# Kernel tuning notes

Measured on AMD Instinct MI355X. Metric: run time of the kernel, lower is better.

The kernel has to match this reference:

```python
import jax, jax.numpy as jnp
import numpy as np

NEG = -1e30  # safe log-zero for fp32/bf16


def _ctc_neg_log_likelihood(labels, log_probs, label_length, data_length, blank):
    """Standard CTC alpha (forward) DP in log space.
    labels: [B, L] int, log_probs: [T, B, C], lengths: [B] int.
    Returns per-example negative log likelihood [B]."""
    T, B, C = log_probs.shape
    L = labels.shape[1]
    S = 2 * L + 1  # extended label: blank, l1, blank, l2, ..., blank
    ext = jnp.full((B, S), blank, dtype=labels.dtype).at[:, 1::2].set(labels)
    prev2 = jnp.concatenate([jnp.full((B, 2), -1, labels.dtype), ext[:, :-2]], axis=1)
    allow_skip = (ext != blank) & (ext != prev2)  # [B, S] skip-transition legality

    def emit(lp_t):  # [B, C] -> [B, S]
        return jnp.take_along_axis(lp_t, ext, axis=1)

    # t = 0: paths can only be at s=0 (blank) or s=1 (first label)
    alpha0 = jnp.where(jnp.arange(S)[None, :] < 2, emit(log_probs[0]), NEG)

    def step(alpha, xs):
        lp_t, t = xs
        a1 = jnp.concatenate([jnp.full((B, 1), NEG, alpha.dtype), alpha[:, :-1]], axis=1)
        a2 = jnp.concatenate([jnp.full((B, 2), NEG, alpha.dtype), alpha[:, :-2]], axis=1)
        a2 = jnp.where(allow_skip, a2, NEG)
        new = jax.nn.logsumexp(jnp.stack([alpha, a1, a2]), axis=0) + emit(lp_t)
        # freeze alpha once past this example's sequence length
        return jnp.where((t < data_length)[:, None], new, alpha), None

    alpha, _ = jax.lax.scan(step, alpha0, (log_probs[1:], jnp.arange(1, T)))

    # likelihood = alpha[2*len] (final blank) + alpha[2*len - 1] (final label)
    a_blank = jnp.take_along_axis(alpha, (2 * label_length)[:, None], axis=1)[:, 0]
    a_label = jnp.take_along_axis(alpha, (2 * label_length - 1)[:, None], axis=1)[:, 0]
    return -jnp.logaddexp(a_blank, a_label)


def setup_inputs() -> dict:
    key = jax.random.key(0)
    k1, k2, k3, k4 = jax.random.split(key, 4)
    T, B, C, L = 1024, 32, 1024, 128
    data = jax.random.normal(k1, (T, B, C), dtype=jnp.float32)
    labels = jax.random.randint(k2, (B, L), 1, C, dtype=jnp.int32)  # avoid blank=0
    label_length = jax.random.randint(k3, (B,), 64, L + 1, dtype=jnp.int32)
    data_length = jax.random.randint(k4, (B,), 512, T + 1, dtype=jnp.int32)
    return {"labels": labels, "data": data, "label_length": label_length,
            "data_length": data_length}


def reference(labels, data, label_length, data_length):
    # from_logits=True -> ctc_loss_v2: log_softmax then CTC; blank_index=0
    log_probs = jax.nn.log_softmax(data, axis=-1)
    loss = _ctc_neg_log_likelihood(labels, log_probs, label_length, data_length, 0)
    return jnp.mean(loss).reshape([1])
```

## Files before the change

kernel.cpp:

```cpp
#include <hip/hip_runtime.h>
#include <hip/hip_bf16.h>

#define T_DIM 1024
#define B_DIM 32
#define C_DIM 1024
#define L_DIM 128
#define S_DIM 257
#define CH    32

#define WS_EPAIR   0
#define WS_LNB     (32u * 1024u * 64u * 8u)
#define WS_ALPHA   (WS_LNB + 32u * 1024u * 4u)
#define WS_BETA    (WS_ALPHA + 32u * 264u * 8u)
#define WS_KACC    (WS_BETA + 32u * 264u * 8u)

__device__ __forceinline__ double lane_shr1_f64(double x) {
#if __has_builtin(__builtin_amdgcn_update_dpp)
    const int lo = __builtin_amdgcn_update_dpp(0, __double2loint(x), 0x138, 0xf, 0xf, true);
    const int hi = __builtin_amdgcn_update_dpp(0, __double2hiint(x), 0x138, 0xf, 0xf, true);
    return __hiloint2double(hi, lo);
#else
    double h = __shfl_up(x, 1, 64);
    return ((threadIdx.x & 63) == 0) ? 0.0 : h;
#endif
}

__global__ __launch_bounds__(256) void emit_kernel(const float* __restrict__ data,
                                                   const int* __restrict__ labels,
                                                   float2* __restrict__ epair,
                                                   float* __restrict__ lnblank) {
    const int wave = threadIdx.x >> 6;
    const int lane = threadIdx.x & 63;
    const int row = blockIdx.x * 4 + wave;
    const int b = row & (B_DIM - 1);
    const int t = row >> 5;

    const float4* d4 = (const float4*)(data + (size_t)row * C_DIM);
    float4 v[4];
    float m = -3.4e38f;
#pragma unroll
    for (int k = 0; k < 4; ++k) {
        v[k] = d4[lane + 64 * k];
        m = fmaxf(m, fmaxf(fmaxf(v[k].x, v[k].y), fmaxf(v[k].z, v[k].w)));
    }
#pragma unroll
    for (int off = 32; off >= 1; off >>= 1)
        m = fmaxf(m, __shfl_xor(m, off, 64));
    float s = 0.f;
#pragma unroll
    for (int k = 0; k < 4; ++k)
        s += __expf(v[k].x - m) + __expf(v[k].y - m) +
             __expf(v[k].z - m) + __expf(v[k].w - m);
#pragma unroll
    for (int off = 32; off >= 1; off >>= 1)
        s += __shfl_xor(s, off, 64);
    const float lse = m + __logf(s);

    const float* drow = data + (size_t)row * C_DIM;
    const float x0 = drow[0];
    const int2 cc = ((const int2*)(labels + b * L_DIM))[lane];
    float2 pr;
    pr.x = __expf(drow[cc.x] - x0);
    pr.y = __expf(drow[cc.y] - x0);
    epair[((size_t)b * T_DIM + t) * 64 + lane] = pr;
    if (lane == 0) lnblank[b * T_DIM + t] = x0 - lse;
}

__global__ __launch_bounds__(64, 1) void dp_kernel(const float2* __restrict__ epair,
                                                   const int* __restrict__ labels,
                                                   const int* __restrict__ label_length,
                                                   const int* __restrict__ data_length,
                                                   double* __restrict__ alphavec,
                                                   double* __restrict__ betavec,
                                                   long long* __restrict__ kaccs) {
    const int b   = blockIdx.x & (B_DIM - 1);
    const int dir = blockIdx.x >> 5;
    const int l = threadIdx.x;
    const int* lab = labels + b * L_DIM;
    const int len = label_length[b];
    const int dlen = data_length[b];
    const int m = dlen >> 1;

    __shared__ float2 ebuf[2][CH][64];

    const float2* eprow = epair + (size_t)b * T_DIM * 64;

    auto stage_chunk = [&](int cb, int trow0) {
#pragma unroll
        for (int i = 0; i < CH / 2; ++i)
            __builtin_amdgcn_global_load_lds(
                (const __attribute__((address_space(1))) void*)
                    ((const char*)(eprow + (size_t)(trow0 + 2 * i) * 64) + l * 16),
                (__attribute__((address_space(3))) void*)(&ebuf[cb][2 * i][0]), 16, 0, 0);
    };

    double a0 = 0.0, a1 = 0.0, a2 = 0.0, a3 = 0.0, a4 = 0.0;
    long long kacc = 0;

    double skip1d, skip3d;
    auto step = [&](double r1, double r3) {
        const double h = lane_shr1_f64(a3);
        const double n0 = a0 + h;
        const double n1 = fma(skip1d, h, a1 + a0) * r1;
        const double n2 = a2 + a1;
        const double n3 = fma(skip3d, a1, a3 + a2) * r3;
        const double n4 = a4 + a3;
        a0 = n0; a1 = n1; a2 = n2; a3 = n3; a4 = n4;
    };

    auto renorm = [&]() {
        double mx = fmax(fmax(fmax(a0, a1), fmax(a2, a3)), a4);
        int hi = __double2hiint(mx);
#pragma unroll
        for (int off = 32; off >= 1; off >>= 1)
            hi = max(hi, __shfl_xor(hi, off, 64));
        const int ex = ((hi >> 20) & 0x7ff) - 1023;
        const double sc = __hiloint2double((1023 - ex) << 20, 0);
        a0 *= sc; a1 *= sc; a2 *= sc; a3 *= sc; a4 *= sc;
        kacc += ex;
    };

    if (dir == 0) {
        const int2 cc = ((const int2*)lab)[l];
        skip1d = ((l > 0) && (cc.x != lab[2 * l - 1])) ? 1.0 : 0.0;
        skip3d = (cc.y != cc.x) ? 1.0 : 0.0;

        stage_chunk(0, 1);
        __builtin_amdgcn_s_waitcnt(0x0f70);

        {
            const float2 ep0 = eprow[l];
            a0 = (l == 0) ? 1.0 : 0.0;
            a1 = (l == 0) ? (double)ep0.x : 0.0;
        }

        const int nsteps = m - 1;
        const int nch = (nsteps + CH - 1) / CH;
        for (int c = 0; c < nch; ++c) {
            const int cb = c & 1;
            const bool more = (c + 1 < nch);
            if (more) stage_chunk(cb ^ 1, 1 + CH * (c + 1));
            __builtin_amdgcn_sched_barrier(0);
            const int t0 = 1 + CH * c;
            if (t0 + CH <= m) {
                double r1R[4], r3R[4];
#pragma unroll
                for (int p = 0; p < 3; ++p) {
                    const float2 ep = ebuf[cb][p][l];
                    r1R[p] = (double)ep.x; r3R[p] = (double)ep.y;
                }
#pragma unroll
                for (int j = 0; j < CH; ++j) {
                    const int jn = (j + 3 < CH) ? (j + 3) : (CH - 1);
                    const float2 epn = ebuf[cb][jn][l];
                    step(r1R[j & 3], r3R[j & 3]);
                    r1R[(j + 3) & 3] = (double)epn.x;
                    r3R[(j + 3) & 3] = (double)epn.y;
                }
            } else {
#pragma unroll
                for (int j = 0; j < CH; ++j) {
                    if (t0 + j < m) {
                        const float2 ep = ebuf[cb][j][l];
                        step((double)ep.x, (double)ep.y);
                    }
                }
            }
            renorm();
            if (more) __builtin_amdgcn_s_waitcnt(0x0f70);
            __builtin_amdgcn_sched_barrier(0);
        }

        double* av = alphavec + b * 264;
        av[4 * l + 0] = a0; av[4 * l + 1] = a1;
        av[4 * l + 2] = a2; av[4 * l + 3] = a3;
        if (l == 63) av[256] = a4;
        if (l == 0) kaccs[2 * b + 0] = kacc;
    } else {
        const int2 c2 = ((const int2*)lab)[63 - l];
        const int labL = (l > 0) ? lab[128 - 2 * l] : -1;
        skip1d = ((l > 0) && (labL != c2.y)) ? 1.0 : 0.0;
        skip3d = (c2.y != c2.x) ? 1.0 : 0.0;

        stage_chunk(0, dlen - 1 - CH);
        __builtin_amdgcn_s_waitcnt(0x0f70);

        {
            const float2 epi = eprow[(size_t)(dlen - 1) * 64 + (63 - l)];
            const int s0 = 256 - 4 * l;
            a0 = (s0 == 2 * len     || s0 == 2 * len - 1) ? 1.0 : 0.0;
            a1 = (s0 - 1 == 2 * len || s0 - 1 == 2 * len - 1) ? (double)epi.y : 0.0;
            a2 = (s0 - 2 == 2 * len || s0 - 2 == 2 * len - 1) ? 1.0 : 0.0;
            a3 = (s0 - 3 == 2 * len || s0 - 3 == 2 * len - 1) ? (double)epi.x : 0.0;
            a4 = 0.0;
        }

        const int nsteps = dlen - 1 - m;
        const int nch = (nsteps + CH - 1) / CH;
        for (int c = 0; c < nch; ++c) {
            const int cb = c & 1;
            const bool more = (c + 1 < nch);
            const int thi = dlen - 2 - CH * c;
            const int tlo = thi - CH + 1;
            if (more) stage_chunk(cb ^ 1, tlo - CH);
            __builtin_amdgcn_sched_barrier(0);
            if (tlo >= m) {
                double r1R[4], r3R[4];
#pragma unroll
                for (int p = 0; p < 3; ++p) {
                    const float2 ep = ebuf[cb][CH - 1 - p][63 - l];
                    r1R[p] = (double)ep.y; r3R[p] = (double)ep.x;
                }
#pragma unroll
                for (int jj = 0; jj < CH; ++jj) {
                    const int jnn = (jj + 3 < CH) ? (jj + 3) : (CH - 1);
                    const float2 epn = ebuf[cb][CH - 1 - jnn][63 - l];
                    step(r1R[jj & 3], r3R[jj & 3]);
                    r1R[(jj + 3) & 3] = (double)epn.y;
                    r3R[(jj + 3) & 3] = (double)epn.x;
                }
            } else {
#pragma unroll
                for (int jj = 0; jj < CH; ++jj) {
                    const int j = CH - 1 - jj;
                    const int t = tlo + j;
                    if (t >= m) {
                        const float2 ep = ebuf[cb][j][63 - l];
                        step((double)ep.y, (double)ep.x);
                    }
                }
            }
            renorm();
            if (more) __builtin_amdgcn_s_waitcnt(0x0f70);
            __builtin_amdgcn_sched_barrier(0);
        }

        double* bv = betavec + b * 264;
        bv[256 - 4 * l] = a0; bv[255 - 4 * l] = a1;
        bv[254 - 4 * l] = a2; bv[253 - 4 * l] = a3;
        if (l == 63) bv[0] = a4;
        if (l == 0) { bv[257] = 0.0; bv[258] = 0.0; kaccs[2 * b + 1] = kacc; }
    }
}

__global__ __launch_bounds__(256) void combine_kernel(const double* __restrict__ alphavec,
                                                      const double* __restrict__ betavec,
                                                      const long long* __restrict__ kaccs,
                                                      const int* __restrict__ labels,
                                                      const int* __restrict__ data_length,
                                                      const float* __restrict__ lnblank,
                                                      float* __restrict__ out) {
    const int wave = threadIdx.x >> 6;
    const int l = threadIdx.x & 63;
    float acc = 0.f;

    for (int b = wave; b < B_DIM; b += 4) {
        const double* A = alphavec + b * 264;
        const double* Bv = betavec + b * 264;
        const int* lab = labels + b * L_DIM;
        const int dlen = data_length[b];

        const double a0 = A[4 * l], a1 = A[4 * l + 1], a2 = A[4 * l + 2], a3 = A[4 * l + 3];
        const double b0 = Bv[4 * l], b1 = Bv[4 * l + 1], b2 = Bv[4 * l + 2];
        const double b3 = Bv[4 * l + 3], b4 = Bv[4 * l + 4], b5 = Bv[4 * l + 5];
        const double sk1 = (lab[2 * l + 1] != lab[2 * l]) ? 1.0 : 0.0;
        const int labn = (l < 63) ? lab[2 * l + 2] : -1;
        const double sk3 = ((l < 63) && (labn != lab[2 * l + 1])) ? 1.0 : 0.0;

        double s = a0 * (b0 + b1)
                 + a1 * (b1 + b2 + sk1 * b3)
                 + a2 * (b2 + b3)
                 + a3 * (b3 + b4 + sk3 * b5);
        if (l == 63) s += A[256] * Bv[256];

        const float* lnb = lnblank + b * T_DIM;
        double slnb = 0.0;
        for (int t = l; t < dlen; t += 64) slnb += (double)lnb[t];

#pragma unroll
        for (int off = 32; off >= 1; off >>= 1) {
            s    += __shfl_xor(s, off, 64);
            slnb += __shfl_xor(slnb, off, 64);
        }

        if (l == 0) {
            const long long k = kaccs[2 * b] + kaccs[2 * b + 1];
            const long long vb = __double_as_longlong(s);
            const int ve = (int)((vb >> 52) & 0x7ff) - 1023;
            const double mant = __longlong_as_double(
                (vb & 0x000FFFFFFFFFFFFFLL) | (1023LL << 52));
            const double l2 = (double)__log2f((float)mant) + (double)ve + (double)k;
            acc += (float)(-(l2 * 0.6931471805599453 + slnb));
        }
    }

    __shared__ float part[4];
    if (l == 0) part[wave] = acc;
    __syncthreads();
    if (threadIdx.x == 0)
        out[0] = (part[0] + part[1] + part[2] + part[3]) * (1.0f / B_DIM);
}

extern "C" void kernel_launch(void* const* d_in, const int* in_sizes, int n_in,
                              void* d_out, int out_size, void* d_ws, size_t ws_size,
                              hipStream_t stream) {
    const int*   labels       = (const int*)d_in[0];
    const float* data         = (const float*)d_in[1];
    const int*   label_length = (const int*)d_in[2];
    const int*   data_length  = (const int*)d_in[3];
    float*       out          = (float*)d_out;

    char* ws = (char*)d_ws;
    float2*    epair    = (float2*)(ws + WS_EPAIR);
    float*     lnblank  = (float*)(ws + WS_LNB);
    double*    alphavec = (double*)(ws + WS_ALPHA);
    double*    betavec  = (double*)(ws + WS_BETA);
    long long* kaccs    = (long long*)(ws + WS_KACC);

    const int rows = T_DIM * B_DIM;
    emit_kernel<<<rows / 4, 256, 0, stream>>>(data, labels, epair, lnblank);
    dp_kernel<<<2 * B_DIM, 64, 0, stream>>>(epair, labels, label_length,
                                            data_length, alphavec, betavec, kaccs);
    combine_kernel<<<1, 256, 0, stream>>>(alphavec, betavec, kaccs, labels,
                                          data_length, lnblank, out);
}
```

Before: 255.4 us.

## Fuse emit and DP kernels with a grid-wide software barrier

Merges the log-softmax/emission kernel and the alpha/beta DP kernel into one persistent launch of 256 blocks. Each wave now processes 32 timesteps for one batch row, and a global atomic-counter barrier separates the emission phase from the DP phase, which only the first 64 blocks run. This removes a kernel launch boundary. It also shrinks the emission grid from 8192 blocks to 256, which lowers parallelism during the memory-bound softmax pass. The DP inner loop is also restructured to load LDS values in groups of four, and a memset is added each call to reset the barrier counter.

```diff
diff --git a/kernel.cpp b/kernel.cpp
--- a/kernel.cpp
+++ b/kernel.cpp
@@ -5,14 +5,15 @@
 #define B_DIM 32
 #define C_DIM 1024
 #define L_DIM 128
-#define S_DIM 257
 #define CH    32
+#define NBLK  256
 
 #define WS_EPAIR   0
 #define WS_LNB     (32u * 1024u * 64u * 8u)
 #define WS_ALPHA   (WS_LNB + 32u * 1024u * 4u)
 #define WS_BETA    (WS_ALPHA + 32u * 264u * 8u)
 #define WS_KACC    (WS_BETA + 32u * 264u * 8u)
+#define WS_BAR     (WS_KACC + 32u * 2u * 8u)
 
 __device__ __forceinline__ double lane_shr1_f64(double x) {
 #if __has_builtin(__builtin_amdgcn_update_dpp)
@@ -25,57 +26,74 @@
 #endif
 }
 
-__global__ __launch_bounds__(256) void emit_kernel(const float* __restrict__ data,
-                                                   const int* __restrict__ labels,
-                                                   float2* __restrict__ epair,
-                                                   float* __restrict__ lnblank) {
-    const int wave = threadIdx.x >> 6;
-    const int lane = threadIdx.x & 63;
-    const int row = blockIdx.x * 4 + wave;
-    const int b = row & (B_DIM - 1);
-    const int t = row >> 5;
-
-    const float4* d4 = (const float4*)(data + (size_t)row * C_DIM);
-    float4 v[4];
-    float m = -3.4e38f;
-#pragma unroll
-    for (int k = 0; k < 4; ++k) {
-        v[k] = d4[lane + 64 * k];
-        m = fmaxf(m, fmaxf(fmaxf(v[k].x, v[k].y), fmaxf(v[k].z, v[k].w)));
+__global__ __launch_bounds__(256, 1) void fused_kernel(const float* __restrict__ data,
+                                                       const int* __restrict__ labels,
+                                                       const int* __restrict__ label_length,
+                                                       const int* __restrict__ data_length,
+                                                       float2* __restrict__ epair,
+                                                       float* __restrict__ lnblank,
+                                                       double* __restrict__ alphavec,
+                                                       double* __restrict__ betavec,
+                                                       long long* __restrict__ kaccs,
+                                                       int* barrier_ct) {
+    const int tid  = threadIdx.x;
+    const int wave = tid >> 6;
+    const int lane = tid & 63;
+
+    {
+        const int gw = blockIdx.x * 4 + wave;
+        const int b  = gw & (B_DIM - 1);
+        const int tb = (gw >> 5) * 32;
+        const int2 cc = ((const int2*)(labels + b * L_DIM))[lane];
+        for (int i = 0; i < 32; ++i) {
+            const int t = tb + i;
+            const size_t row = (size_t)t * B_DIM + b;
+            const float4* d4 = (const float4*)(data + row * C_DIM);
+            float4 v[4];
+            float mx = -3.4e38f;
+#pragma unroll
+            for (int k = 0; k < 4; ++k) {
+                v[k] = d4[lane + 64 * k];
+                mx = fmaxf(mx, fmaxf(fmaxf(v[k].x, v[k].y), fmaxf(v[k].z, v[k].w)));
+            }
+#pragma unroll
+            for (int off = 32; off >= 1; off >>= 1)
+                mx = fmaxf(mx, __shfl_xor(mx, off, 64));
+            float s = 0.f;
+#pragma unroll
+            for (int k = 0; k < 4; ++k)
+                s += __expf(v[k].x - mx) + __expf(v[k].y - mx) +
+                     __expf(v[k].z - mx) + __expf(v[k].w - mx);
+#pragma unroll
+            for (int off = 32; off >= 1; off >>= 1)
+                s += __shfl_xor(s, off, 64);
+            const float lse = mx + __logf(s);
+
+            const float* drow = data + row * C_DIM;
+            const float x0 = drow[0];
+            float2 pr;
+            pr.x = __expf(drow[cc.x] - x0);
+            pr.y = __expf(drow[cc.y] - x0);
+            epair[((size_t)b * T_DIM + t) * 64 + lane] = pr;
+            if (lane == 0) lnblank[b * T_DIM + t] = x0 - lse;
+        }
     }
-#pragma unroll
-    for (int off = 32; off >= 1; off >>= 1)
-        m = fmaxf(m, __shfl_xor(m, off, 64));
-    float s = 0.f;
-#pragma unroll
-    for (int k = 0; k < 4; ++k)
-        s += __expf(v[k].x - m) + __expf(v[k].y - m) +
-             __expf(v[k].z - m) + __expf(v[k].w - m);
-#pragma unroll
-    for (int off = 32; off >= 1; off >>= 1)
-        s += __shfl_xor(s, off, 64);
-    const float lse = m + __logf(s);
-
-    const float* drow = data + (size_t)row * C_DIM;
-    const float x0 = drow[0];
-    const int2 cc = ((const int2*)(labels + b * L_DIM))[lane];
-    float2 pr;
-    pr.x = __expf(drow[cc.x] - x0);
-    pr.y = __expf(drow[cc.y] - x0);
-    epair[((size_t)b * T_DIM + t) * 64 + lane] = pr;
-    if (lane == 0) lnblank[b * T_DIM + t] = x0 - lse;
-}
-
-__global__ __launch_bounds__(64, 1) void dp_kernel(const float2* __restrict__ epair,
-                                                   const int* __restrict__ labels,
-                                                   const int* __restrict__ label_length,
-                                                   const int* __restrict__ data_length,
-                                                   double* __restrict__ alphavec,
-                                                   double* __restrict__ betavec,
-                                                   long long* __restrict__ kaccs) {
+
+    __threadfence();
+    __syncthreads();
+    if (tid == 0) {
+        atomicAdd(barrier_ct, 1);
+        while (atomicAdd(barrier_ct, 0) < NBLK)
+            __builtin_amdgcn_s_sleep(2);
+        __threadfence();
+    }
+    __syncthreads();
+
+    if (blockIdx.x >= 2 * B_DIM || tid >= 64) return;
+
     const int b   = blockIdx.x & (B_DIM - 1);
     const int dir = blockIdx.x >> 5;
-    const int l = threadIdx.x;
+    const int l = lane;
     const int* lab = labels + b * L_DIM;
     const int len = label_length[b];
     const int dlen = data_length[b];
@@ -143,19 +161,21 @@
             __builtin_amdgcn_sched_barrier(0);
             const int t0 = 1 + CH * c;
             if (t0 + CH <= m) {
-                double r1R[4], r3R[4];
-#pragma unroll
-                for (int p = 0; p < 3; ++p) {
-                    const float2 ep = ebuf[cb][p][l];
-                    r1R[p] = (double)ep.x; r3R[p] = (double)ep.y;
-                }
-#pragma unroll
-                for (int j = 0; j < CH; ++j) {
-                    const int jn = (j + 3 < CH) ? (j + 3) : (CH - 1);
-                    const float2 epn = ebuf[cb][jn][l];
-                    step(r1R[j & 3], r3R[j & 3]);
-                    r1R[(j + 3) & 3] = (double)epn.x;
-                    r3R[(j + 3) & 3] = (double)epn.y;
+                double c0x, c0y, c1x, c1y, c2x, c2y, c3x, c3y;
+                {
+                    const float2 e0 = ebuf[cb][0][l], e1 = ebuf[cb][1][l];
+                    const float2 e2 = ebuf[cb][2][l], e3 = ebuf[cb][3][l];
+                    c0x = e0.x; c0y = e0.y; c1x = e1.x; c1y = e1.y;
+                    c2x = e2.x; c2y = e2.y; c3x = e3.x; c3y = e3.y;
+                }
+#pragma unroll
+                for (int g = 0; g < 8; ++g) {
+                    const int jn = (g < 7) ? (4 * g + 4) : 28;
+                    const float2 f0 = ebuf[cb][jn + 0][l], f1 = ebuf[cb][jn + 1][l];
+                    const float2 f2 = ebuf[cb][jn + 2][l], f3 = ebuf[cb][jn + 3][l];
+                    step(c0x, c0y); step(c1x, c1y); step(c2x, c2y); step(c3x, c3y);
+                    c0x = f0.x; c0y = f0.y; c1x = f1.x; c1y = f1.y;
+                    c2x = f2.x; c2y = f2.y; c3x = f3.x; c3y = f3.y;
                 }
             } else {
 #pragma unroll
@@ -205,19 +225,21 @@
             if (more) stage_chunk(cb ^ 1, tlo - CH);
             __builtin_amdgcn_sched_barrier(0);
             if (tlo >= m) {
-                double r1R[4], r3R[4];
-#pragma unroll
-                for (int p = 0; p < 3; ++p) {
-                    const float2 ep = ebuf[cb][CH - 1 - p][63 - l];
-                    r1R[p] = (double)ep.y; r3R[p] = (double)ep.x;
-                }
-#pragma unroll
-                for (int jj = 0; jj < CH; ++jj) {
-                    const int jnn = (jj + 3 < CH) ? (jj + 3) : (CH - 1);
-                    const float2 epn = ebuf[cb][CH - 1 - jnn][63 - l];
-                    step(r1R[jj & 3], r3R[jj & 3]);
-                    r1R[(jj + 3) & 3] = (double)epn.y;
-                    r3R[(jj + 3) & 3] = (double)epn.x;
+                double c0x, c0y, c1x, c1y, c2x, c2y, c3x, c3y;
+                {
+                    const float2 e0 = ebuf[cb][31][63 - l], e1 = ebuf[cb][30][63 - l];
+                    const float2 e2 = ebuf[cb][29][63 - l], e3 = ebuf[cb][28][63 - l];
+                    c0x = e0.y; c0y = e0.x; c1x = e1.y; c1y = e1.x;
+                    c2x = e2.y; c2y = e2.x; c3x = e3.y; c3y = e3.x;
+                }
+#pragma unroll
+                for (int g = 0; g < 8; ++g) {
+                    const int jb = (g < 7) ? (27 - 4 * g) : 3;
+                    const float2 f0 = ebuf[cb][jb - 0][63 - l], f1 = ebuf[cb][jb - 1][63 - l];
+                    const float2 f2 = ebuf[cb][jb - 2][63 - l], f3 = ebuf[cb][jb - 3][63 - l];
+                    step(c0x, c0y); step(c1x, c1y); step(c2x, c2y); step(c3x, c3y);
+                    c0x = f0.y; c0y = f0.x; c1x = f1.y; c1y = f1.x;
+                    c2x = f2.y; c2y = f2.x; c3x = f3.y; c3y = f3.x;
                 }
             } else {
 #pragma unroll
@@ -316,11 +338,11 @@
     double*    alphavec = (double*)(ws + WS_ALPHA);
     double*    betavec  = (double*)(ws + WS_BETA);
     long long* kaccs    = (long long*)(ws + WS_KACC);
-
-    const int rows = T_DIM * B_DIM;
-    emit_kernel<<<rows / 4, 256, 0, stream>>>(data, labels, epair, lnblank);
-    dp_kernel<<<2 * B_DIM, 64, 0, stream>>>(epair, labels, label_length,
-                                            data_length, alphavec, betavec, kaccs);
+    int*       bar      = (int*)(ws + WS_BAR);
+
+    hipMemsetAsync(bar, 0, sizeof(int), stream);
+    fused_kernel<<<NBLK, 256, 0, stream>>>(data, labels, label_length, data_length,
+                                           epair, lnblank, alphavec, betavec, kaccs, bar);
     combine_kernel<<<1, 256, 0, stream>>>(alphavec, betavec, kaccs, labels,
                                           data_length, lnblank, out);
 }
```

New measurement: 323.6 us. +26.7%, slower.
